# Optimization experiments

Hardware: AMD Instinct MI355X
Metric: run time of the kernel (lower is better)

Reference implementation:

```python
import jax, jax.numpy as jnp
import numpy as np

NUM_HEADS = 16
LN_EPS = 1e-5

def _layernorm(x, g, b):
    m = jnp.mean(x, axis=-1, keepdims=True)
    v = jnp.var(x, axis=-1, keepdims=True)
    return (x - m) * jax.lax.rsqrt(v + LN_EPS) * g + b

def _mha(xq, xkv, qw, qb, kw, kb, vw, vb, ow, ob, causal):
    B, T, D = xq.shape
    S = xkv.shape[1]
    Hd = D // NUM_HEADS
    q = (xq @ qw + qb).reshape(B, T, NUM_HEADS, Hd)
    k = (xkv @ kw + kb).reshape(B, S, NUM_HEADS, Hd)
    v = (xkv @ vw + vb).reshape(B, S, NUM_HEADS, Hd)
    scores = jnp.einsum('bthd,bshd->bhts', q, k) / np.sqrt(Hd).astype(np.float32)
    if causal:
        mask = jnp.arange(T)[:, None] >= jnp.arange(S)[None, :]
        scores = jnp.where(mask, scores, jnp.float32(-jnp.inf))
    attn = jax.nn.softmax(scores, axis=-1)
    out = jnp.einsum('bhts,bshd->bthd', attn, v).reshape(B, T, D)
    return out @ ow + ob

def setup_inputs() -> dict:
    B, T, S, D, F = 4, 2048, 2048, 1024, 4096
    key = jax.random.key(0)
    ks = jax.random.split(key, 16)
    w = lambda k, shape: jax.random.normal(k, shape, dtype=jnp.float32) * 0.02
    z = lambda n: jnp.zeros((n,), jnp.float32)
    o = lambda n: jnp.ones((n,), jnp.float32)
    return {
        'x': jax.random.normal(ks[0], (B, T, D), dtype=jnp.float32),
        'encoder_output': jax.random.normal(ks[1], (B, S, D), dtype=jnp.float32),
        'sa_qw': w(ks[2], (D, D)), 'sa_qb': z(D),
        'sa_kw': w(ks[3], (D, D)), 'sa_kb': z(D),
        'sa_vw': w(ks[4], (D, D)), 'sa_vb': z(D),
        'sa_ow': w(ks[5], (D, D)), 'sa_ob': z(D),
        'ca_qw': w(ks[6], (D, D)), 'ca_qb': z(D),
        'ca_kw': w(ks[7], (D, D)), 'ca_kb': z(D),
        'ca_vw': w(ks[8], (D, D)), 'ca_vb': z(D),
        'ca_ow': w(ks[9], (D, D)), 'ca_ob': z(D),
        'ff_w1': w(ks[10], (D, F)), 'ff_b1': z(F),
        'ff_w2': w(ks[11], (F, D)), 'ff_b2': z(D),
        'ln1_g': o(D), 'ln1_b': z(D),
        'ln2_g': o(D), 'ln2_b': z(D),
        'ln3_g': o(D), 'ln3_b': z(D),
    }

def reference(x, encoder_output,
              sa_qw, sa_qb, sa_kw, sa_kb, sa_vw, sa_vb, sa_ow, sa_ob,
              ca_qw, ca_qb, ca_kw, ca_kb, ca_vw, ca_vb, ca_ow, ca_ob,
              ff_w1, ff_b1, ff_w2, ff_b2,
              ln1_g, ln1_b, ln2_g, ln2_b, ln3_g, ln3_b):
    # pre-norm causal self-attn + residual
    h = _layernorm(x, ln1_g, ln1_b)
    x = x + _mha(h, h, sa_qw, sa_qb, sa_kw, sa_kb, sa_vw, sa_vb, sa_ow, sa_ob, causal=True)
    # pre-norm cross-attn + residual
    h = _layernorm(x, ln2_g, ln2_b)
    x = x + _mha(h, encoder_output, ca_qw, ca_qb, ca_kw, ca_kb, ca_vw, ca_vb, ca_ow, ca_ob, causal=False)
    # pre-norm FFN + residual (dropout = identity in eval)
    h = _layernorm(x, ln3_g, ln3_b)
    x = x + (jax.nn.relu(h @ ff_w1 + ff_b1) @ ff_w2 + ff_b2)
    return x
```

## Files before the change

### kernel.cpp

```cpp
#include <hip/hip_runtime.h>
#include <stdint.h>

#define D_MODEL 1024
#define D_FF    4096
#define NHEADS  16
#define HD      64
#define LN_EPS  1e-5f

using u16 = unsigned short;
typedef __bf16 bf16x8 __attribute__((ext_vector_type(8)));
typedef float  f32x4  __attribute__((ext_vector_type(4)));
typedef float  f32x16 __attribute__((ext_vector_type(16)));

typedef __attribute__((address_space(1))) uint32_t as1_u32;
typedef __attribute__((address_space(3))) uint32_t as3_u32;

__device__ __forceinline__ u16 f2bf(float f) {
  union { float f; uint32_t u; } v; v.f = f;
  uint32_t r = v.u + 0x7FFFu + ((v.u >> 16) & 1u);
  return (u16)(r >> 16);
}

__device__ __forceinline__ uint32_t cvtpk(float lo, float hi) {
  uint32_t r;
  asm("v_cvt_pk_bf16_f32 %0, %1, %2" : "=v"(r) : "v"(lo), "v"(hi));
  return r;
}

__device__ __forceinline__ void gl_lds16(const void* g, void* l) {
  __builtin_amdgcn_global_load_lds((const as1_u32*)(uintptr_t)g,
                                   (as3_u32*)(uint32_t)(uintptr_t)l, 16, 0, 0);
}

__global__ __launch_bounds__(256)
void transpose_cast(const float* __restrict__ W, u16* __restrict__ Wt, int K, int N) {
  __shared__ float t[32][33];
  const int k0 = blockIdx.x * 32, n0 = blockIdx.y * 32;
  const int x = threadIdx.x & 31, y = threadIdx.x >> 5;
#pragma unroll
  for (int j = 0; j < 32; j += 8)
    t[y + j][x] = W[(size_t)(k0 + y + j) * N + (n0 + x)];
  __syncthreads();
#pragma unroll
  for (int j = 0; j < 32; j += 8)
    Wt[(size_t)(n0 + y + j) * K + (k0 + x)] = f2bf(t[x][y + j]);
}

struct Src8 { const float* s[8]; };
__global__ __launch_bounds__(256)
void transpose_cast8(Src8 p, u16* __restrict__ dstbase) {
  __shared__ float t[32][33];
  const float* __restrict__ W = p.s[blockIdx.z];
  u16* __restrict__ Wt = dstbase + (size_t)blockIdx.z * (1024 * 1024);
  const int k0 = blockIdx.x * 32, n0 = blockIdx.y * 32;
  const int x = threadIdx.x & 31, y = threadIdx.x >> 5;
#pragma unroll
  for (int j = 0; j < 32; j += 8)
    t[y + j][x] = W[(size_t)(k0 + y + j) * 1024 + (n0 + x)];
  __syncthreads();
#pragma unroll
  for (int j = 0; j < 32; j += 8)
    Wt[(size_t)(n0 + y + j) * 1024 + (k0 + x)] = f2bf(t[x][y + j]);
}

__global__ __launch_bounds__(256)
void cast_f32_bf16(const float* __restrict__ in, u16* __restrict__ out, int n4) {
  int i = blockIdx.x * 256 + threadIdx.x;
  if (i < n4) {
    float4 v = ((const float4*)in)[i];
    ushort4 o;
    o.x = f2bf(v.x); o.y = f2bf(v.y); o.z = f2bf(v.z); o.w = f2bf(v.w);
    ((ushort4*)out)[i] = o;
  }
}

__global__ __launch_bounds__(256)
void ln_bf16(const float* __restrict__ x, const float* __restrict__ g,
             const float* __restrict__ bta, u16* __restrict__ out) {
  const int row = blockIdx.x;
  const int tid = threadIdx.x;
  const float4 v = ((const float4*)(x + (size_t)row * D_MODEL))[tid];
  float s  = v.x + v.y + v.z + v.w;
  float s2 = v.x * v.x + v.y * v.y + v.z * v.z + v.w * v.w;
#pragma unroll
  for (int off = 1; off < 64; off <<= 1) {
    s  += __shfl_xor(s, off);
    s2 += __shfl_xor(s2, off);
  }
  __shared__ float sm[8];
  const int wave = tid >> 6, lane = tid & 63;
  if (lane == 0) { sm[wave] = s; sm[4 + wave] = s2; }
  __syncthreads();
  s  = sm[0] + sm[1] + sm[2] + sm[3];
  s2 = sm[4] + sm[5] + sm[6] + sm[7];
  const float mean = s * (1.f / D_MODEL);
  const float var  = s2 * (1.f / D_MODEL) - mean * mean;
  const float rstd = rsqrtf(var + LN_EPS);
  const float4 gv = ((const float4*)g)[tid];
  const float4 bv = ((const float4*)bta)[tid];
  ushort4 o;
  o.x = f2bf((v.x - mean) * rstd * gv.x + bv.x);
  o.y = f2bf((v.y - mean) * rstd * gv.y + bv.y);
  o.z = f2bf((v.z - mean) * rstd * gv.z + bv.z);
  o.w = f2bf((v.w - mean) * rstd * gv.w + bv.w);
  ((ushort4*)(out + (size_t)row * D_MODEL))[tid] = o;
}

#define QSCALE 0.18033688011112042f
template<int EPI>
__global__ __launch_bounds__(256, 3)
void gemm_bf16(const u16* __restrict__ A, const u16* __restrict__ Wt,
               const float* __restrict__ bias, const float* __restrict__ bias2,
               const float* __restrict__ bias3, const float* resid,
               u16* __restrict__ outb, u16* __restrict__ outb2, u16* __restrict__ outb3,
               float* outf, int M, int N, int K) {
  __shared__ u16 lA[128 * 32];
  __shared__ u16 lB[128 * 32];
  const int tid  = threadIdx.x;
  const int lane = tid & 63;
  const int wave = tid >> 6;
  const int wr = wave >> 1, wc = wave & 1;
  const int lr = lane & 15, lg = lane >> 4;
  const int row0 = blockIdx.x * 128, col0 = blockIdx.y * 128;

  const char* pa = (const char*)A  + ((size_t)(row0 + (tid >> 2)) * K + (size_t)(tid & 3) * 8) * 2;
  const char* pb = (const char*)Wt + ((size_t)(col0 + (tid >> 2)) * K + (size_t)(tid & 3) * 8) * 2;
  const size_t rowskip = (size_t)64 * K * 2;
  char* la = (char*)lA + wave * 1024;
  char* lb = (char*)lB + wave * 1024;

  f32x4 acc[4][4] = {};
  const int ksteps = K >> 5;
  for (int kt = 0; kt < ksteps; ++kt) {
    gl_lds16(pa, la);
    gl_lds16(pa + rowskip, la + 4096);
    gl_lds16(pb, lb);
    gl_lds16(pb + rowskip, lb + 4096);
    pa += 64; pb += 64;
    __syncthreads();
    bf16x8 af[4], bfr[4];
#pragma unroll
    for (int m = 0; m < 4; ++m)
      af[m] = *(const bf16x8*)((const char*)lA + (wr * 64 + m * 16 + lr) * 64 + lg * 16);
#pragma unroll
    for (int n = 0; n < 4; ++n)
      bfr[n] = *(const bf16x8*)((const char*)lB + (wc * 64 + n * 16 + lr) * 64 + lg * 16);
#pragma unroll
    for (int m = 0; m < 4; ++m)
#pragma unroll
      for (int n = 0; n < 4; ++n)
        acc[m][n] = __builtin_amdgcn_mfma_f32_16x16x32_bf16(af[m], bfr[n], acc[m][n], 0, 0, 0);
    __syncthreads();
  }

#pragma unroll
  for (int m = 0; m < 4; ++m) {
    const int grow = row0 + wr * 64 + m * 16 + lg * 4;
#pragma unroll
    for (int n = 0; n < 4; ++n) {
      const int gcol = col0 + wc * 64 + n * 16 + lr;
      if (EPI == 4 || EPI == 5) {
        const int seg = gcol >> 10;
        const int c = gcol & 1023;
        const bool isV = (EPI == 4) ? (seg == 2) : (seg == 1);
        if (isV) {
          const float bv = (EPI == 4 ? bias3 : bias2)[c];
          const int hh = c >> 6, dd = c & 63;
          const int bb = grow >> 11, tt = grow & 2047;
          u16* vT = (EPI == 4) ? outb3 : outb2;
          uint2 st;
          st.x = cvtpk(acc[m][n][0] + bv, acc[m][n][1] + bv);
          st.y = cvtpk(acc[m][n][2] + bv, acc[m][n][3] + bv);
          *(uint2*)(vT + (((size_t)(bb * NHEADS + hh) * 64 + dd) << 11) + tt) = st;
        } else {
          const float bv = ((EPI == 4) ? ((seg == 0) ? bias : bias2) : bias)[c];
          const float sc = (EPI == 4 && seg == 0) ? QSCALE : 1.f;
          u16* optr = (EPI == 4) ? ((seg == 0) ? outb : outb2) : outb;
#pragma unroll
          for (int r = 0; r < 4; ++r)
            optr[(size_t)(grow + r) * 1024 + c] = f2bf((acc[m][n][r] + bv) * sc);
        }
      } else {
        const float bv = bias[gcol];
#pragma unroll
        for (int r = 0; r < 4; ++r) {
          float v = acc[m][n][r] + bv;
          if (EPI == 0)      outb[(size_t)(grow + r) * N + gcol] = f2bf(v);
          else if (EPI == 1) outb[(size_t)(grow + r) * N + gcol] = f2bf(v > 0.f ? v : 0.f);
          else if (EPI == 3) outb[(size_t)(grow + r) * N + gcol] = f2bf(v * QSCALE);
          else {
            const size_t idx = (size_t)(grow + r) * N + gcol;
            outf[idx] = v + resid[idx];
          }
        }
      }
    }
  }
}

template<bool CAUSAL>
__global__ __launch_bounds__(256, 4)
void attn_kernel(const u16* __restrict__ Q, const u16* __restrict__ Kb,
                 const u16* __restrict__ Vt, u16* __restrict__ O,
                 int T, int S) {
  __shared__ u16 lQ[128 * 64];
  __shared__ u16 lK[64 * 64];
  __shared__ u16 lVt[64 * 64];

  const int f  = blockIdx.x;
  const int bh = f & 63;
  const int b = bh >> 4, hd = bh & 15;
  const int qx = f >> 6;
  const int q0 = (CAUSAL ? (T / 128 - 1 - qx) : qx) * 128;
  const int tid = threadIdx.x, lane = tid & 63, wave = tid >> 6;
  const int l31 = lane & 31, hb = lane >> 5;

  const u16* Qbase = Q  + (size_t)(b * T) * D_MODEL + hd * HD;
  const u16* Kbase = Kb + (size_t)(b * S) * D_MODEL + hd * HD;
  const u16* Vbase = Vt + ((size_t)(b * NHEADS + hd) << 17);
  const size_t rskip = (size_t)32 * D_MODEL * 2;

  const int srow = tid >> 3;
  const int sg   = (tid & 7) ^ (srow & 7);
  const int sgv0 = (tid & 7) ^ ((srow >> 3) & 7);
  const int sgv1 = sgv0 ^ 4;
  const int sprow = (srow & ~12) | ((srow & 4) << 1) | ((srow & 8) >> 1);

  {
    const char* src = (const char*)(Qbase + (size_t)(q0 + srow) * D_MODEL) + sg * 16;
    char* dst = (char*)lQ + wave * 1024;
    gl_lds16(src,             dst);
    gl_lds16(src + rskip,     dst + 4096);
    gl_lds16(src + 2 * rskip, dst + 8192);
    gl_lds16(src + 3 * rskip, dst + 12288);
  }

  bf16x8 qf[4];
  f32x16 oacc0 = {}, oacc1 = {};
  float m_run = -1e30f, l_run = 0.f;
  const int qq = q0 + wave * 32 + l31;

  const int ktEnd = CAUSAL ? (q0 / 64 + 2) : (S / 64);

  for (int kt = 0; kt < ktEnd; ++kt) {
    {
      const char* src = (const char*)(Kbase + (size_t)(kt * 64 + sprow) * D_MODEL) + sg * 16;
      char* dst = (char*)lK + wave * 1024;
      gl_lds16(src, dst);
      gl_lds16(src + rskip, dst + 4096);
    }
    {
      const char* srcv = (const char*)(Vbase + ((size_t)srow << 11) + kt * 64);
      char* dst = (char*)lVt + wave * 1024;
      gl_lds16(srcv + sgv0 * 16, dst);
      gl_lds16(srcv + (32u << 12) + sgv1 * 16, dst + 4096);
    }
    __syncthreads();

    if (kt == 0) {
      const int qrow = wave * 32 + l31;
#pragma unroll
      for (int dc = 0; dc < 4; ++dc)
        qf[dc] = *(const bf16x8*)((const char*)lQ + qrow * 128 +
                                  (((2 * dc + hb) ^ (qrow & 7)) << 4));
    }

    const bool live = !CAUSAL || (kt * 64 <= q0 + wave * 32 + 31);
    if (live) {
      f32x16 z0 = {}, z1 = {};
      __builtin_amdgcn_s_setprio(1);
#pragma unroll
      for (int dc = 0; dc < 4; ++dc) {
        bf16x8 kf0 = *(const bf16x8*)((const char*)lK + l31 * 128 +
                                      (((2 * dc + hb) ^ (l31 & 7)) << 4));
        z0 = __builtin_amdgcn_mfma_f32_32x32x16_bf16(kf0, qf[dc], z0, 0, 0, 0);
      }
#pragma unroll
      for (int dc = 0; dc < 4; ++dc) {
        bf16x8 kf1 = *(const bf16x8*)((const char*)lK + (32 + l31) * 128 +
                                      (((2 * dc + hb) ^ (l31 & 7)) << 4));
        z1 = __builtin_amdgcn_mfma_f32_32x32x16_bf16(kf1, qf[dc], z1, 0, 0, 0);
      }
      __builtin_amdgcn_s_setprio(0);

      if (CAUSAL && kt * 64 + 63 > q0 + wave * 32) {
        const int kvb = kt * 64 + 8 * hb;
#pragma unroll
        for (int r = 0; r < 16; ++r) {
          const int kv = kvb + (r & 7) + 16 * (r >> 3);
          if (kv > qq)      z0[r] = -1e30f;
          if (kv + 32 > qq) z1[r] = -1e30f;
        }
      }

      float t[16];
#pragma unroll
      for (int r = 0; r < 16; ++r) t[r] = fmaxf(z0[r], z1[r]);
#pragma unroll
      for (int sdt = 8; sdt >= 1; sdt >>= 1)
#pragma unroll
        for (int i = 0; i < 8; ++i)
          if (i < sdt) t[i] = fmaxf(t[i], t[i + sdt]);
      float mx = t[0];
      mx = fmaxf(mx, __shfl_xor(mx, 32));

      if (!__all(mx - m_run <= 11.5f)) {
        const float mn = fmaxf(m_run, mx);
        const float scl = exp2f(m_run - mn);
        m_run = mn;
        l_run *= scl;
#pragma unroll
        for (int r = 0; r < 16; ++r) { oacc0[r] *= scl; oacc1[r] *= scl; }
      }
      float sum = 0.f;
#pragma unroll
      for (int r = 0; r < 16; ++r) {
        z0[r] = exp2f(z0[r] - m_run); sum += z0[r];
        z1[r] = exp2f(z1[r] - m_run); sum += z1[r];
      }
      sum += __shfl_xor(sum, 32);
      l_run += sum;

      bf16x8 pf[4];
      {
        union { uint32_t u[4]; bf16x8 v; } w0, w1, w2, w3;
#pragma unroll
        for (int i = 0; i < 4; ++i) {
          w0.u[i] = cvtpk(z0[2 * i],     z0[2 * i + 1]);
          w1.u[i] = cvtpk(z0[8 + 2 * i], z0[9 + 2 * i]);
          w2.u[i] = cvtpk(z1[2 * i],     z1[2 * i + 1]);
          w3.u[i] = cvtpk(z1[8 + 2 * i], z1[9 + 2 * i]);
        }
        pf[0] = w0.v; pf[1] = w1.v; pf[2] = w2.v; pf[3] = w3.v;
      }

      __builtin_amdgcn_s_setprio(1);
#pragma unroll
      for (int c = 0; c < 4; ++c) {
        bf16x8 vf0 = *(const bf16x8*)((const char*)lVt + l31 * 128 +
                       (((2 * c + hb) ^ ((l31 >> 3) & 7)) << 4));
        oacc0 = __builtin_amdgcn_mfma_f32_32x32x16_bf16(vf0, pf[c], oacc0, 0, 0, 0);
        bf16x8 vf1 = *(const bf16x8*)((const char*)lVt + (32 + l31) * 128 +
                       ((((2 * c + hb) ^ (((32 + l31) >> 3) & 7))) << 4));
        oacc1 = __builtin_amdgcn_mfma_f32_32x32x16_bf16(vf1, pf[c], oacc1, 0, 0, 0);
      }
      __builtin_amdgcn_s_setprio(0);
    }
    __syncthreads();
  }

  const float linv = 1.f / l_run;
  u16* Op = O + (size_t)(b * T + qq) * D_MODEL + hd * HD + 4 * hb;
#pragma unroll
  for (int rr = 0; rr < 4; ++rr) {
    uint2 st0, st1;
    st0.x = cvtpk(oacc0[4 * rr + 0] * linv, oacc0[4 * rr + 1] * linv);
    st0.y = cvtpk(oacc0[4 * rr + 2] * linv, oacc0[4 * rr + 3] * linv);
    *(uint2*)(Op + 8 * rr) = st0;
    st1.x = cvtpk(oacc1[4 * rr + 0] * linv, oacc1[4 * rr + 1] * linv);
    st1.y = cvtpk(oacc1[4 * rr + 2] * linv, oacc1[4 * rr + 3] * linv);
    *(uint2*)(Op + 32 + 8 * rr) = st1;
  }
}

extern "C" void kernel_launch(void* const* d_in, const int* in_sizes, int n_in,
                              void* d_out, int out_size, void* d_ws, size_t ws_size,
                              hipStream_t stream) {
  (void)in_sizes; (void)n_in; (void)out_size; (void)ws_size;
  const int B = 4, T = 2048, S = 2048, Dm = 1024, F = 4096;
  const int M = B * T;

  const float* x   = (const float*)d_in[0];
  const float* enc = (const float*)d_in[1];

  char* p = (char*)d_ws;
  auto take = [&](size_t bytes) { char* r = p; p += (bytes + 255) & ~(size_t)255; return r; };
  u16* wt8  = (u16*)take((size_t)8 * Dm * Dm * 2);
  u16* ff1T = (u16*)take((size_t)F * Dm * 2);
  u16* ff2T = (u16*)take((size_t)Dm * F * 2);
  u16*   h    = (u16*)take((size_t)M * Dm * 2);
  u16*   encb = (u16*)take((size_t)M * Dm * 2);
  float* xc   = (float*)take((size_t)M * Dm * 4);
  char*  Dreg = take((size_t)M * F * 2);
  u16* qb = (u16*)Dreg;
  u16* kb = (u16*)(Dreg + (size_t)M * Dm * 2);
  u16* vb = (u16*)(Dreg + (size_t)2 * M * Dm * 2);
  u16* ab = (u16*)(Dreg + (size_t)3 * M * Dm * 2);
  u16* ffmid = (u16*)Dreg;

  dim3 blk(256);
  Src8 s8 = {{ (const float*)d_in[2], (const float*)d_in[4], (const float*)d_in[6],
               (const float*)d_in[8], (const float*)d_in[10], (const float*)d_in[12],
               (const float*)d_in[14], (const float*)d_in[16] }};
  transpose_cast8<<<dim3(32, 32, 8), blk, 0, stream>>>(s8, wt8);
  transpose_cast<<<dim3(Dm / 32, F / 32), blk, 0, stream>>>((const float*)d_in[18], ff1T, Dm, F);
  transpose_cast<<<dim3(F / 32, Dm / 32), blk, 0, stream>>>((const float*)d_in[20], ff2T, F, Dm);
  cast_f32_bf16<<<dim3((M * Dm / 4) / 256), blk, 0, stream>>>(enc, encb, M * Dm / 4);

  dim3 gproj(M / 128, Dm / 128);
  dim3 gqkv(M / 128, 3072 / 128);
  dim3 gkv(M / 128, 2048 / 128);
  dim3 gffn1(M / 128, F / 128);
  dim3 gattn((T / 128) * 64);

  ln_bf16<<<M, blk, 0, stream>>>(x, (const float*)d_in[22], (const float*)d_in[23], h);
  gemm_bf16<4><<<gqkv, blk, 0, stream>>>(h, wt8,
      (const float*)d_in[3], (const float*)d_in[5], (const float*)d_in[7],
      nullptr, qb, kb, vb, nullptr, M, 3072, Dm);
  attn_kernel<true><<<gattn, blk, 0, stream>>>(qb, kb, vb, ab, T, S);
  gemm_bf16<2><<<gproj, blk, 0, stream>>>(ab, wt8 + (size_t)3 * Dm * Dm,
      (const float*)d_in[9], nullptr, nullptr, x, nullptr, nullptr, nullptr, xc, M, Dm, Dm);

  ln_bf16<<<M, blk, 0, stream>>>(xc, (const float*)d_in[24], (const float*)d_in[25], h);
  gemm_bf16<3><<<gproj, blk, 0, stream>>>(h, wt8 + (size_t)4 * Dm * Dm,
      (const float*)d_in[11], nullptr, nullptr, nullptr, qb, nullptr, nullptr, nullptr, M, Dm, Dm);
  gemm_bf16<5><<<gkv, blk, 0, stream>>>(encb, wt8 + (size_t)5 * Dm * Dm,
      (const float*)d_in[13], (const float*)d_in[15], nullptr,
      nullptr, kb, vb, nullptr, nullptr, M, 2048, Dm);
  attn_kernel<false><<<gattn, blk, 0, stream>>>(qb, kb, vb, ab, T, S);
  gemm_bf16<2><<<gproj, blk, 0, stream>>>(ab, wt8 + (size_t)7 * Dm * Dm,
      (const float*)d_in[17], nullptr, nullptr, xc, nullptr, nullptr, nullptr, xc, M, Dm, Dm);

  ln_bf16<<<M, blk, 0, stream>>>(xc, (const float*)d_in[26], (const float*)d_in[27], h);
  gemm_bf16<1><<<gffn1, blk, 0, stream>>>(h, ff1T, (const float*)d_in[19],
      nullptr, nullptr, nullptr, ffmid, nullptr, nullptr, nullptr, M, F, Dm);
  gemm_bf16<2><<<gproj, blk, 0, stream>>>(ffmid, ff2T, (const float*)d_in[21],
      nullptr, nullptr, xc, nullptr, nullptr, nullptr, (float*)d_out, M, Dm, F);
}
```

Before: 642.1 us.

## Store residual stream in bf16 and remap GEMM blocks for XCD locality

The intermediate residual stream moves from fp32 to bf16 buffers, so the projection epilogues and layernorm kernels read and write half the bytes. New epilogue variants add bf16 residuals, and layernorm gains a bf16-input template. The GEMM grid also becomes 1D, with a block-index remap that spreads tiles across the 8 XCDs so neighbouring tiles share L2. This trades accuracy, since the residual is rounded to bf16 twice, and the remap assumes the grid size is a multiple of 8.

```diff
diff --git a/kernel.cpp b/kernel.cpp
--- a/kernel.cpp
+++ b/kernel.cpp
@@ -19,6 +19,10 @@
   union { float f; uint32_t u; } v; v.f = f;
   uint32_t r = v.u + 0x7FFFu + ((v.u >> 16) & 1u);
   return (u16)(r >> 16);
+}
+
+__device__ __forceinline__ float bf2f(u16 u) {
+  union { uint32_t u; float f; } v; v.u = (uint32_t)u << 16; return v.f;
 }
 
 __device__ __forceinline__ uint32_t cvtpk(float lo, float hi) {
@@ -74,12 +78,20 @@
   }
 }
 
+template<int BF16IN>
 __global__ __launch_bounds__(256)
-void ln_bf16(const float* __restrict__ x, const float* __restrict__ g,
-             const float* __restrict__ bta, u16* __restrict__ out) {
+void ln_bf16(const float* __restrict__ xf, const u16* __restrict__ xb,
+             const float* __restrict__ g, const float* __restrict__ bta,
+             u16* __restrict__ out) {
   const int row = blockIdx.x;
   const int tid = threadIdx.x;
-  const float4 v = ((const float4*)(x + (size_t)row * D_MODEL))[tid];
+  float4 v;
+  if (BF16IN) {
+    ushort4 u = ((const ushort4*)(xb + (size_t)row * D_MODEL))[tid];
+    v.x = bf2f(u.x); v.y = bf2f(u.y); v.z = bf2f(u.z); v.w = bf2f(u.w);
+  } else {
+    v = ((const float4*)(xf + (size_t)row * D_MODEL))[tid];
+  }
   float s  = v.x + v.y + v.z + v.w;
   float s2 = v.x * v.x + v.y * v.y + v.z * v.z + v.w * v.w;
 #pragma unroll
@@ -111,7 +123,8 @@
 __global__ __launch_bounds__(256, 3)
 void gemm_bf16(const u16* __restrict__ A, const u16* __restrict__ Wt,
                const float* __restrict__ bias, const float* __restrict__ bias2,
-               const float* __restrict__ bias3, const float* resid,
+               const float* __restrict__ bias3,
+               const float* __restrict__ residf, const u16* __restrict__ residb,
                u16* __restrict__ outb, u16* __restrict__ outb2, u16* __restrict__ outb3,
                float* outf, int M, int N, int K) {
   __shared__ u16 lA[128 * 32];
@@ -121,7 +134,12 @@
   const int wave = tid >> 6;
   const int wr = wave >> 1, wc = wave & 1;
   const int lr = lane & 15, lg = lane >> 4;
-  const int row0 = blockIdx.x * 128, col0 = blockIdx.y * 128;
+
+  const int cpx = gridDim.x >> 3;
+  const int wg  = (blockIdx.x & 7) * cpx + (blockIdx.x >> 3);
+  const int gx  = M >> 7;
+  const int row0 = (wg % gx) << 7;
+  const int col0 = (wg / gx) << 7;
 
   const char* pa = (const char*)A  + ((size_t)(row0 + (tid >> 2)) * K + (size_t)(tid & 3) * 8) * 2;
   const char* pb = (const char*)Wt + ((size_t)(col0 + (tid >> 2)) * K + (size_t)(tid & 3) * 8) * 2;
@@ -184,14 +202,14 @@
         const float bv = bias[gcol];
 #pragma unroll
         for (int r = 0; r < 4; ++r) {
+          const size_t idx = (size_t)(grow + r) * N + gcol;
           float v = acc[m][n][r] + bv;
-          if (EPI == 0)      outb[(size_t)(grow + r) * N + gcol] = f2bf(v);
-          else if (EPI == 1) outb[(size_t)(grow + r) * N + gcol] = f2bf(v > 0.f ? v : 0.f);
-          else if (EPI == 3) outb[(size_t)(grow + r) * N + gcol] = f2bf(v * QSCALE);
-          else {
-            const size_t idx = (size_t)(grow + r) * N + gcol;
-            outf[idx] = v + resid[idx];
-          }
+          if (EPI == 0)      outb[idx] = f2bf(v);
+          else if (EPI == 1) outb[idx] = f2bf(v > 0.f ? v : 0.f);
+          else if (EPI == 2) outb[idx] = f2bf(v + residf[idx]);
+          else if (EPI == 3) outb[idx] = f2bf(v * QSCALE);
+          else if (EPI == 6) outb[idx] = f2bf(v + bf2f(residb[idx]));
+          else               outf[idx] = v + bf2f(residb[idx]);
         }
       }
     }
@@ -380,7 +398,8 @@
   u16* ff2T = (u16*)take((size_t)Dm * F * 2);
   u16*   h    = (u16*)take((size_t)M * Dm * 2);
   u16*   encb = (u16*)take((size_t)M * Dm * 2);
-  float* xc   = (float*)take((size_t)M * Dm * 4);
+  u16*   xc   = (u16*)take((size_t)M * Dm * 2);
+  u16*   xc2  = (u16*)take((size_t)M * Dm * 2);
   char*  Dreg = take((size_t)M * F * 2);
   u16* qb = (u16*)Dreg;
   u16* kb = (u16*)(Dreg + (size_t)M * Dm * 2);
@@ -397,33 +416,33 @@
   transpose_cast<<<dim3(F / 32, Dm / 32), blk, 0, stream>>>((const float*)d_in[20], ff2T, F, Dm);
   cast_f32_bf16<<<dim3((M * Dm / 4) / 256), blk, 0, stream>>>(enc, encb, M * Dm / 4);
 
-  dim3 gproj(M / 128, Dm / 128);
-  dim3 gqkv(M / 128, 3072 / 128);
-  dim3 gkv(M / 128, 2048 / 128);
-  dim3 gffn1(M / 128, F / 128);
+  const int gproj = (M / 128) * (1024 / 128);
+  const int gqkv  = (M / 128) * (3072 / 128);
+  const int gkv   = (M / 128) * (2048 / 128);
+  const int gffn1 = (M / 128) * (4096 / 128);
   dim3 gattn((T / 128) * 64);
 
-  ln_bf16<<<M, blk, 0, stream>>>(x, (const float*)d_in[22], (const float*)d_in[23], h);
+  ln_bf16<0><<<M, blk, 0, stream>>>(x, nullptr, (const float*)d_in[22], (const float*)d_in[23], h);
   gemm_bf16<4><<<gqkv, blk, 0, stream>>>(h, wt8,
       (const float*)d_in[3], (const float*)d_in[5], (const float*)d_in[7],
-      nullptr, qb, kb, vb, nullptr, M, 3072, Dm);
+      nullptr, nullptr, qb, kb, vb, nullptr, M, 3072, Dm);
   attn_kernel<true><<<gattn, blk, 0, stream>>>(qb, kb, vb, ab, T, S);
   gemm_bf16<2><<<gproj, blk, 0, stream>>>(ab, wt8 + (size_t)3 * Dm * Dm,
-      (const float*)d_in[9], nullptr, nullptr, x, nullptr, nullptr, nullptr, xc, M, Dm, Dm);
-
-  ln_bf16<<<M, blk, 0, stream>>>(xc, (const float*)d_in[24], (const float*)d_in[25], h);
+      (const float*)d_in[9], nullptr, nullptr, x, nullptr, xc, nullptr, nullptr, nullptr, M, Dm, Dm);
+
+  ln_bf16<1><<<M, blk, 0, stream>>>(nullptr, xc, (const float*)d_in[24], (const float*)d_in[25], h);
   gemm_bf16<3><<<gproj, blk, 0, stream>>>(h, wt8 + (size_t)4 * Dm * Dm,
-      (const float*)d_in[11], nullptr, nullptr, nullptr, qb, nullptr, nullptr, nullptr, M, Dm, Dm);
+      (const float*)d_in[11], nullptr, nullptr, nullptr, nullptr, qb, nullptr, nullptr, nullptr, M, Dm, Dm);
   gemm_bf16<5><<<gkv, blk, 0, stream>>>(encb, wt8 + (size_t)5 * Dm * Dm,
       (const float*)d_in[13], (const float*)d_in[15], nullptr,
-      nullptr, kb, vb, nullptr, nullptr, M, 2048, Dm);
+      nullptr, nullptr, kb, vb, nullptr, nullptr, M, 2048, Dm);
   attn_kernel<false><<<gattn, blk, 0, stream>>>(qb, kb, vb, ab, T, S);
-  gemm_bf16<2><<<gproj, blk, 0, stream>>>(ab, wt8 + (size_t)7 * Dm * Dm,
-      (const float*)d_in[17], nullptr, nullptr, xc, nullptr, nullptr, nullptr, xc, M, Dm, Dm);
-
-  ln_bf16<<<M, blk, 0, stream>>>(xc, (const float*)d_in[26], (const float*)d_in[27], h);
+  gemm_bf16<6><<<gproj, blk, 0, stream>>>(ab, wt8 + (size_t)7 * Dm * Dm,
+      (const float*)d_in[17], nullptr, nullptr, nullptr, xc, xc2, nullptr, nullptr, nullptr, M, Dm, Dm);
+
+  ln_bf16<1><<<M, blk, 0, stream>>>(nullptr, xc2, (const float*)d_in[26], (const float*)d_in[27], h);
   gemm_bf16<1><<<gffn1, blk, 0, stream>>>(h, ff1T, (const float*)d_in[19],
-      nullptr, nullptr, nullptr, ffmid, nullptr, nullptr, nullptr, M, F, Dm);
-  gemm_bf16<2><<<gproj, blk, 0, stream>>>(ffmid, ff2T, (const float*)d_in[21],
-      nullptr, nullptr, xc, nullptr, nullptr, nullptr, (float*)d_out, M, Dm, F);
-}
+      nullptr, nullptr, nullptr, nullptr, ffmid, nullptr, nullptr, nullptr, M, F, Dm);
+  gemm_bf16<7><<<gproj, blk, 0, stream>>>(ffmid, ff2T, (const float*)d_in[21],
+      nullptr, nullptr, nullptr, xc2, nullptr, nullptr, nullptr, (float*)d_out, M, Dm, F);
+}
```

Measured after the change: 664.2 us. 1.03x slower.
